# Kernel tuning notes

Measured on AMD Instinct MI355X. Metric: run time of the kernel, lower is better.

Reference implementation:

```python
import jax, jax.numpy as jnp
import numpy as np

HEADS = 8
DIM_HEAD = 32
DIM = 256           # must equal HEADS*DIM_HEAD (required by the torch view)
HIDDEN = HEADS * DIM_HEAD
NUM_GROUPS = 32
EPS = 1e-6


def setup_inputs() -> dict:
    key = jax.random.key(0)
    ks = jax.random.split(key, 6)
    b, c, h, w = 16, DIM, 64, 64
    x = jax.random.normal(ks[0], (b, c, h, w), dtype=jnp.float32)
    # conv1x1 weights stored as 2D matrices (out_ch, in_ch)
    w_qkv = jax.random.normal(ks[1], (3 * HIDDEN, DIM), dtype=jnp.float32) * (1.0 / np.sqrt(DIM))
    w_out = jax.random.normal(ks[2], (DIM, HIDDEN), dtype=jnp.float32) * (1.0 / np.sqrt(HIDDEN))
    b_out = jax.random.normal(ks[3], (DIM,), dtype=jnp.float32) * 0.01
    gn_gamma = jnp.ones((DIM,), dtype=jnp.float32)
    gn_beta = jnp.zeros((DIM,), dtype=jnp.float32)
    return {"x": x, "w_qkv": w_qkv, "w_out": w_out, "b_out": b_out,
            "gn_gamma": gn_gamma, "gn_beta": gn_beta}


def _group_norm(x, gamma, beta):
    # GroupNorm32: compute in float32, eps=1e-6, affine
    b, c, h, w = x.shape
    g = NUM_GROUPS
    xf = x.astype(jnp.float32).reshape(b, g, c // g, h, w)
    mean = xf.mean(axis=(2, 3, 4), keepdims=True)
    var = xf.var(axis=(2, 3, 4), keepdims=True)
    xn = (xf - mean) * jax.lax.rsqrt(var + EPS)
    xn = xn.reshape(b, c, h, w)
    return (xn * gamma[None, :, None, None] + beta[None, :, None, None]).astype(x.dtype)


def reference(x, w_qkv, w_out, b_out, gn_gamma, gn_beta):
    b, c, h, w = x.shape
    n = h * w
    # qkv projection (1x1 conv == matmul over channels)
    qkv = jnp.einsum('oc,bchw->bohw', w_qkv, x)            # (b, 3*hidden, h, w)
    qkv = qkv.reshape(b, 3, HEADS, DIM_HEAD, n)
    q, k, v = qkv[:, 0], qkv[:, 1], qkv[:, 2]              # (b, h, d, n)
    q = jax.nn.softmax(q, axis=-2)                         # softmax over feature dim
    k = jax.nn.softmax(k, axis=-1)                         # softmax over spatial dim
    context = jnp.einsum('bhdn,bhen->bhde', k, v)          # (b, heads, d, d)
    out = jnp.einsum('bhde,bhdn->bhen', context, q)        # (b, heads, d, n)
    out = out.reshape(b, c, h, w)
    out = jnp.einsum('oc,bchw->bohw', w_out, out) + b_out[None, :, None, None]
    out = _group_norm(out, gn_gamma, gn_beta)
    return out + x
```

## Files before the change

kernel.cpp:

```cpp
#include <hip/hip_runtime.h>


typedef short s8v __attribute__((ext_vector_type(8)));
typedef float f32x4 __attribute__((ext_vector_type(4)));

__device__ __forceinline__ short f2bf(float f) {
  union { float f; unsigned u; } v; v.f = f;
  unsigned r = v.u + 0x7FFF + ((v.u >> 16) & 1);
  return (short)(r >> 16);
}
__device__ __forceinline__ short f2bf_t(float f) {
  union { float f; unsigned u; } v; v.f = f;
  return (short)(v.u >> 16);
}
__device__ __forceinline__ float bf2f(short h) {
  union { unsigned u; float f; } v; v.u = ((unsigned)(unsigned short)h) << 16;
  return v.f;
}
__device__ __forceinline__ void gld16(const short* g, short* l) {
  __builtin_amdgcn_global_load_lds(
      (const __attribute__((address_space(1))) unsigned*)g,
      (__attribute__((address_space(3))) unsigned*)l, 16, 0, 0);
}

__global__ __launch_bounds__(256) void prep(
    const float* __restrict__ x, short* __restrict__ xt,
    const float* __restrict__ wsrc, short* __restrict__ wdst,
    float* __restrict__ st2) {
  int t = threadIdx.x;
  if (blockIdx.z == 16) {
    int slot = blockIdx.y * 64 + blockIdx.x;
    if (slot < 96) {
      int id = slot * 256 + t;
      long off = (long)id * 8;
      float4 a = *(const float4*)&wsrc[off];
      float4 b = *(const float4*)&wsrc[off + 4];
      s8v o;
      o[0] = f2bf(a.x); o[1] = f2bf(a.y); o[2] = f2bf(a.z); o[3] = f2bf(a.w);
      o[4] = f2bf(b.x); o[5] = f2bf(b.y); o[6] = f2bf(b.z); o[7] = f2bf(b.w);
      *(s8v*)&wdst[off] = o;
    } else if (slot == 96) {
      float4 z = {0.f, 0.f, 0.f, 0.f};
      ((float4*)st2)[t] = z;
    }
    return;
  }
  int b = blockIdx.z;
  int n0 = blockIdx.x * 64, c0 = blockIdx.y * 64;
  __shared__ short ls[64][65];
  const float* xb = x + ((long)b * 256 + c0) * 4096 + n0;
  int ci = t >> 4, j4 = (t & 15) * 4;
#pragma unroll
  for (int i = 0; i < 4; ++i) {
    int cl = ci + i * 16;
    float4 v = *(const float4*)&xb[(long)cl * 4096 + j4];
    ls[j4 + 0][cl] = f2bf(v.x);
    ls[j4 + 1][cl] = f2bf(v.y);
    ls[j4 + 2][cl] = f2bf(v.z);
    ls[j4 + 3][cl] = f2bf(v.w);
  }
  __syncthreads();
  short* xtb = xt + ((long)b * 4096 + n0) * 256 + c0;
#pragma unroll
  for (int i = 0; i < 2; ++i) {
    int id = t + i * 256;
    int nl = id >> 3, c8 = (id & 7) * 8;
    s8v o;
#pragma unroll
    for (int e = 0; e < 8; ++e) o[e] = ls[nl][c8 + e];
    *(s8v*)&xtb[(long)nl * 256 + c8] = o;
  }
}

__global__ __launch_bounds__(256) void gemm_qkv(
    const short* __restrict__ A, const short* __restrict__ Bt,
    short* __restrict__ kv, short* __restrict__ qT) {
  __shared__ short lA[8192];
  __shared__ short lB[8192];
  int b = blockIdx.z;
  int mt = blockIdx.y * 128, nt = blockIdx.x * 128;
  int tid = threadIdx.x;
  int lane = tid & 63;
  int wm = tid >> 7, wn = (tid >> 6) & 1;
  int rl = lane & 15, kg = lane >> 4;
  const short* Ab = A + (long)mt * 256;
  const short* Bb = Bt + ((long)b * 4096 + nt) * 256;

  f32x4 acc[4][4];
#pragma unroll
  for (int i = 0; i < 4; ++i)
#pragma unroll
    for (int j = 0; j < 4; ++j) acc[i][j] = (f32x4){0.f, 0.f, 0.f, 0.f};

  for (int k0 = 0; k0 < 256; k0 += 64) {
#pragma unroll
    for (int is = 0; is < 4; ++is) {
      int s = is * 256 + tid;
      int row = s >> 3, kcp = s & 7;
      int kcl = kcp ^ (row & 7);
      gld16(Ab + (long)row * 256 + k0 + kcl * 8, &lA[(is * 256 + (tid & ~63)) * 8]);
      gld16(Bb + (long)row * 256 + k0 + kcl * 8, &lB[(is * 256 + (tid & ~63)) * 8]);
    }
    asm volatile("s_waitcnt vmcnt(0)" ::: "memory");
    __syncthreads();
#pragma unroll
    for (int kw = 0; kw < 2; ++kw) {
      int kc = kw * 4 + kg;
      s8v av[4], bv[4];
#pragma unroll
      for (int mi = 0; mi < 4; ++mi) {
        int row = wm * 64 + mi * 16 + rl;
        av[mi] = *(const s8v*)&lA[row * 64 + ((kc ^ (row & 7)) << 3)];
      }
#pragma unroll
      for (int ni = 0; ni < 4; ++ni) {
        int row = wn * 64 + ni * 16 + rl;
        bv[ni] = *(const s8v*)&lB[row * 64 + ((kc ^ (row & 7)) << 3)];
      }
#pragma unroll
      for (int mi = 0; mi < 4; ++mi)
#pragma unroll
        for (int ni = 0; ni < 4; ++ni)
          acc[mi][ni] = __builtin_amdgcn_mfma_f32_16x16x32_bf16(
              av[mi], bv[ni], acc[mi][ni], 0, 0, 0);
    }
    __syncthreads();
  }

  if (mt < 256) {
    short* qTb = qT + ((long)b * 4096 + nt) * 256 + mt;
#pragma unroll
    for (int ni = 0; ni < 4; ++ni) {
      int n = wn * 64 + ni * 16 + rl;
#pragma unroll
      for (int p = 0; p < 2; ++p) {
        float v[8];
        float m = -1e30f;
#pragma unroll
        for (int j = 0; j < 8; ++j) {
          v[j] = acc[p * 2 + (j >> 2)][ni][j & 3];
          m = fmaxf(m, v[j]);
        }
        m = fmaxf(m, __shfl_xor(m, 16));
        m = fmaxf(m, __shfl_xor(m, 32));
        float ssum = 0.f;
#pragma unroll
        for (int j = 0; j < 8; ++j) { v[j] = __expf(v[j] - m); ssum += v[j]; }
        ssum += __shfl_xor(ssum, 16);
        ssum += __shfl_xor(ssum, 32);
        float inv = 1.f / ssum;
#pragma unroll
        for (int half = 0; half < 2; ++half) {
          short4 o;
          o.x = f2bf_t(v[half * 4 + 0] * inv);
          o.y = f2bf_t(v[half * 4 + 1] * inv);
          o.z = f2bf_t(v[half * 4 + 2] * inv);
          o.w = f2bf_t(v[half * 4 + 3] * inv);
          *(short4*)&qTb[(long)n * 256 + wm * 64 + p * 32 + half * 16 + kg * 4] = o;
        }
      }
    }
  } else {
    short* Cb = kv + ((long)b * 512 + (mt - 256)) * 4096 + nt;
#pragma unroll
    for (int mi = 0; mi < 4; ++mi) {
#pragma unroll
      for (int r = 0; r < 4; ++r) {
        int o = wm * 64 + mi * 16 + kg * 4 + r;
#pragma unroll
        for (int ni = 0; ni < 4; ++ni) {
          int n = wn * 64 + ni * 16 + rl;
          Cb[(long)o * 4096 + n] = f2bf(acc[mi][ni][r]);
        }
      }
    }
  }
}

__global__ __launch_bounds__(256) void gemm_lin(
    const short* __restrict__ A, const short* __restrict__ Bt,
    short* __restrict__ C, const float* __restrict__ bias,
    float* __restrict__ st2) {
  __shared__ short lA[8192];
  __shared__ short lB[8192];
  int b = blockIdx.z;
  int mt = blockIdx.y * 128, nt = blockIdx.x * 128;
  int tid = threadIdx.x;
  int lane = tid & 63;
  int wm = tid >> 7, wn = (tid >> 6) & 1;
  int rl = lane & 15, kg = lane >> 4;
  const short* Ab = A + (long)b * 65536 + (long)mt * 256;
  const short* Bb = Bt + ((long)b * 4096 + nt) * 256;

  f32x4 acc[4][4];
#pragma unroll
  for (int i = 0; i < 4; ++i)
#pragma unroll
    for (int j = 0; j < 4; ++j) acc[i][j] = (f32x4){0.f, 0.f, 0.f, 0.f};

  for (int k0 = 0; k0 < 256; k0 += 64) {
#pragma unroll
    for (int is = 0; is < 4; ++is) {
      int s = is * 256 + tid;
      int row = s >> 3, kcp = s & 7;
      int kcl = kcp ^ (row & 7);
      gld16(Ab + (long)row * 256 + k0 + kcl * 8, &lA[(is * 256 + (tid & ~63)) * 8]);
      gld16(Bb + (long)row * 256 + k0 + kcl * 8, &lB[(is * 256 + (tid & ~63)) * 8]);
    }
    asm volatile("s_waitcnt vmcnt(0)" ::: "memory");
    __syncthreads();
#pragma unroll
    for (int kw = 0; kw < 2; ++kw) {
      int kc = kw * 4 + kg;
      s8v av[4], bv[4];
#pragma unroll
      for (int mi = 0; mi < 4; ++mi) {
        int row = wm * 64 + mi * 16 + rl;
        av[mi] = *(const s8v*)&lA[row * 64 + ((kc ^ (row & 7)) << 3)];
      }
#pragma unroll
      for (int ni = 0; ni < 4; ++ni) {
        int row = wn * 64 + ni * 16 + rl;
        bv[ni] = *(const s8v*)&lB[row * 64 + ((kc ^ (row & 7)) << 3)];
      }
#pragma unroll
      for (int mi = 0; mi < 4; ++mi)
#pragma unroll
        for (int ni = 0; ni < 4; ++ni)
          acc[mi][ni] = __builtin_amdgcn_mfma_f32_16x16x32_bf16(
              av[mi], bv[ni], acc[mi][ni], 0, 0, 0);
    }
    __syncthreads();
  }

  short* Cb = C + ((long)b * 256 + mt) * 4096 + nt;
  float s1[4] = {0.f, 0.f, 0.f, 0.f};
  float s2[4] = {0.f, 0.f, 0.f, 0.f};
#pragma unroll
  for (int mi = 0; mi < 4; ++mi) {
#pragma unroll
    for (int r = 0; r < 4; ++r) {
      int o = wm * 64 + mi * 16 + kg * 4 + r;
      float bv = bias[mt + o];
#pragma unroll
      for (int ni = 0; ni < 4; ++ni) {
        int n = wn * 64 + ni * 16 + rl;
        short h = f2bf(acc[mi][ni][r] + bv);
        Cb[(long)o * 4096 + n] = h;
        float q = bf2f(h);
        s1[mi] += q;
        s2[mi] += q * q;
      }
    }
  }
#pragma unroll
  for (int mi = 0; mi < 4; ++mi) {
#pragma unroll
    for (int off = 1; off <= 16; off <<= 1) {
      s1[mi] += __shfl_xor(s1[mi], off);
      s2[mi] += __shfl_xor(s2[mi], off);
    }
    if (rl == 0 && (kg & 1) == 0) {
      int g = (mt >> 3) + wm * 8 + mi * 2 + (kg >> 1);
      atomicAdd(&st2[(b * 32 + g) * 2], s1[mi]);
      atomicAdd(&st2[(b * 32 + g) * 2 + 1], s2[mi]);
    }
  }
}

__global__ __launch_bounds__(256) void ctx_mfma(
    const short* __restrict__ kv, float* __restrict__ ctxp, float* __restrict__ sp) {
  int split = blockIdx.x;
  int h = blockIdx.y, b = blockIdx.z;
  int tid = threadIdx.x;
  int w = tid >> 6, l = tid & 63;
  const short* kb = kv + ((long)(b * 512) + h * 32) * 4096;
  const short* vb = kb + (long)256 * 4096;
  int rl = l & 15, kg = l >> 4;
  int n_base = split * 1024 + w * 256;

  f32x4 acc[2][2];
#pragma unroll
  for (int i = 0; i < 2; ++i)
#pragma unroll
    for (int j = 0; j < 2; ++j) acc[i][j] = (f32x4){0.f, 0.f, 0.f, 0.f};
  float s_part0 = 0.f, s_part1 = 0.f;

#pragma unroll 2
  for (int it = 0; it < 8; ++it) {
    int n0 = n_base + it * 32 + kg * 8;
    s8v a0, a1, b0, b1;
    {
      s8v kr = *(const s8v*)&kb[(long)rl * 4096 + n0];
#pragma unroll
      for (int j = 0; j < 8; ++j) {
        float f = __expf(bf2f(kr[j]));
        s_part0 += f;
        a0[j] = f2bf_t(f);
      }
    }
    {
      s8v kr = *(const s8v*)&kb[(long)(16 + rl) * 4096 + n0];
#pragma unroll
      for (int j = 0; j < 8; ++j) {
        float f = __expf(bf2f(kr[j]));
        s_part1 += f;
        a1[j] = f2bf_t(f);
      }
    }
    b0 = *(const s8v*)&vb[(long)rl * 4096 + n0];
    b1 = *(const s8v*)&vb[(long)(16 + rl) * 4096 + n0];
    acc[0][0] = __builtin_amdgcn_mfma_f32_16x16x32_bf16(a0, b0, acc[0][0], 0, 0, 0);
    acc[0][1] = __builtin_amdgcn_mfma_f32_16x16x32_bf16(a0, b1, acc[0][1], 0, 0, 0);
    acc[1][0] = __builtin_amdgcn_mfma_f32_16x16x32_bf16(a1, b0, acc[1][0], 0, 0, 0);
    acc[1][1] = __builtin_amdgcn_mfma_f32_16x16x32_bf16(a1, b1, acc[1][1], 0, 0, 0);
  }
  s_part0 += __shfl_xor(s_part0, 16); s_part0 += __shfl_xor(s_part0, 32);
  s_part1 += __shfl_xor(s_part1, 16); s_part1 += __shfl_xor(s_part1, 32);

  __shared__ float lctx[4][1024];
  __shared__ float lsum[4][32];
#pragma unroll
  for (int di = 0; di < 2; ++di)
#pragma unroll
    for (int ei = 0; ei < 2; ++ei)
#pragma unroll
      for (int r = 0; r < 4; ++r) {
        int row = di * 16 + kg * 4 + r;
        int col = ei * 16 + rl;
        lctx[w][row * 32 + col] = acc[di][ei][r];
      }
  if (kg == 0) { lsum[w][rl] = s_part0; lsum[w][16 + rl] = s_part1; }
  __syncthreads();
  long base = (long)(b * 8 + h) * 4 + split;
#pragma unroll
  for (int i = 0; i < 4; ++i) {
    int id = tid + i * 256;
    ctxp[base * 1024 + id] = lctx[0][id] + lctx[1][id] + lctx[2][id] + lctx[3][id];
  }
  if (tid < 32)
    sp[base * 32 + tid] = lsum[0][tid] + lsum[1][tid] + lsum[2][tid] + lsum[3][tid];
}

__global__ __launch_bounds__(256) void make_wf(
    const float* __restrict__ ctxp, const float* __restrict__ sp,
    const float* __restrict__ w_out, short* __restrict__ wf) {
  int h = blockIdx.x, b = blockIdx.y;
  __shared__ float c[32][33];
  __shared__ float inv_s[32];
  __shared__ float wv[256][33];
  int t = threadIdx.x;
  long base = (long)(b * 8 + h) * 4;
#pragma unroll
  for (int i = 0; i < 4; ++i) {
    int id = t + i * 256;
    float v = ctxp[base * 1024 + id] + ctxp[(base + 1) * 1024 + id] +
              ctxp[(base + 2) * 1024 + id] + ctxp[(base + 3) * 1024 + id];
    c[id >> 5][id & 31] = v;
  }
  if (t < 32) {
    float sv = sp[base * 32 + t] + sp[(base + 1) * 32 + t] +
               sp[(base + 2) * 32 + t] + sp[(base + 3) * 32 + t];
    inv_s[t] = 1.f / sv;
  }
#pragma unroll
  for (int r = 0; r < 32; ++r) {
    int row = r * 8 + (t >> 5);
    wv[row][t & 31] = w_out[row * 256 + h * 32 + (t & 31)];
  }
  __syncthreads();
  float wr[32];
#pragma unroll
  for (int e = 0; e < 32; ++e) wr[e] = wv[t][e];
  float tmp[32];
#pragma unroll
  for (int dd = 0; dd < 32; ++dd) {
    float sum = 0.f;
#pragma unroll
    for (int e = 0; e < 32; ++e) sum += wr[e] * c[dd][e];
    tmp[dd] = sum * inv_s[dd];
  }
  short* dst = wf + ((long)b * 256 + t) * 256 + h * 32;
#pragma unroll
  for (int c8 = 0; c8 < 4; ++c8) {
    s8v o;
#pragma unroll
    for (int e = 0; e < 8; ++e) o[e] = f2bf(tmp[c8 * 8 + e]);
    *(s8v*)&dst[c8 * 8] = o;
  }
}

__global__ __launch_bounds__(256) void final_out(
    const short* __restrict__ lin, const float* __restrict__ x,
    const float2* __restrict__ st2, const float* __restrict__ gamma,
    const float* __restrict__ beta, float* __restrict__ out) {
  long id = (long)blockIdx.x * 256 + threadIdx.x;
  long e0 = id * 8;
  int b = (int)(e0 >> 20);
  int rem = (int)(e0 & 1048575);
  int c = rem >> 12;
  float2 st = st2[b * 32 + (c >> 3)];
  float mean = st.x * (1.f / 32768.f);
  float inv = rsqrtf(st.y * (1.f / 32768.f) - mean * mean + 1e-6f);
  float ga = gamma[c] * inv;
  float be = beta[c] - mean * ga;
  s8v l8 = __builtin_nontemporal_load((const s8v*)&lin[e0]);
  f32x4 x0 = __builtin_nontemporal_load((const f32x4*)&x[e0]);
  f32x4 x1 = __builtin_nontemporal_load((const f32x4*)&x[e0 + 4]);
  f32x4 o0, o1;
  o0[0] = bf2f(l8[0]) * ga + be + x0[0];
  o0[1] = bf2f(l8[1]) * ga + be + x0[1];
  o0[2] = bf2f(l8[2]) * ga + be + x0[2];
  o0[3] = bf2f(l8[3]) * ga + be + x0[3];
  o1[0] = bf2f(l8[4]) * ga + be + x1[0];
  o1[1] = bf2f(l8[5]) * ga + be + x1[1];
  o1[2] = bf2f(l8[6]) * ga + be + x1[2];
  o1[3] = bf2f(l8[7]) * ga + be + x1[3];
  __builtin_nontemporal_store(o0, (f32x4*)&out[e0]);
  __builtin_nontemporal_store(o1, (f32x4*)&out[e0 + 4]);
}

extern "C" void kernel_launch(void* const* d_in, const int* in_sizes, int n_in,
                              void* d_out, int out_size, void* d_ws, size_t ws_size,
                              hipStream_t stream) {
  const float* x     = (const float*)d_in[0];
  const float* w_qkv = (const float*)d_in[1];
  const float* w_out = (const float*)d_in[2];
  const float* b_out = (const float*)d_in[3];
  const float* gamma = (const float*)d_in[4];
  const float* beta  = (const float*)d_in[5];
  float* out = (float*)d_out;

  short* xt   = (short*)d_ws;
  short* qT   = xt + 16777216;
  short* kvb  = qT + 16777216;
  short* lin  = kvb + 33554432;
  short* wqb  = lin + 16777216;
  short* wfb  = wqb + 196608;
  float* ctxp = (float*)(wfb + 1048576);
  float* sp   = ctxp + 524288;
  float* st2  = sp + 16384;

  prep<<<dim3(64, 4, 17), 256, 0, stream>>>(x, xt, w_qkv, wqb, st2);
  gemm_qkv<<<dim3(32, 6, 16), 256, 0, stream>>>(wqb, xt, kvb, qT);
  ctx_mfma<<<dim3(4, 8, 16), 256, 0, stream>>>(kvb, ctxp, sp);
  make_wf<<<dim3(8, 16), 256, 0, stream>>>(ctxp, sp, w_out, wfb);
  gemm_lin<<<dim3(32, 2, 16), 256, 0, stream>>>(wfb, qT, lin, b_out, st2);
  final_out<<<8192, 256, 0, stream>>>(lin, x, (const float2*)st2, gamma, beta, out);
}
```

Before: 145.9 us.

## Fuse make_wf into ctx_mfma via last-block-done atomic counter

Removes the separate make_wf launch by having the last of the four split blocks per (batch, head) in ctx_mfma perform the context reduction and the weight fold. Completion is detected with a per-head atomic counter that prep zeroes, with thread fences around it. This saves one kernel launch and its gap, at the cost of a larger shared-memory footprint in ctx_mfma (about 38 KB) and a serialized tail on the last block.

```diff
diff --git a/kernel.cpp b/kernel.cpp
--- a/kernel.cpp
+++ b/kernel.cpp
@@ -26,7 +26,7 @@
 __global__ __launch_bounds__(256) void prep(
     const float* __restrict__ x, short* __restrict__ xt,
     const float* __restrict__ wsrc, short* __restrict__ wdst,
-    float* __restrict__ st2) {
+    float* __restrict__ st2, int* __restrict__ cnt) {
   int t = threadIdx.x;
   if (blockIdx.z == 16) {
     int slot = blockIdx.y * 64 + blockIdx.x;
@@ -42,6 +42,7 @@
     } else if (slot == 96) {
       float4 z = {0.f, 0.f, 0.f, 0.f};
       ((float4*)st2)[t] = z;
+      if (t < 32) ((float4*)cnt)[t] = z;
     }
     return;
   }
@@ -269,7 +270,10 @@
 }
 
 __global__ __launch_bounds__(256) void ctx_mfma(
-    const short* __restrict__ kv, float* __restrict__ ctxp, float* __restrict__ sp) {
+    const short* __restrict__ kv, float* __restrict__ ctxp, float* __restrict__ sp,
+    const float* __restrict__ w_out, short* __restrict__ wf, int* __restrict__ cnt) {
+  __shared__ float sh[9536];
+  __shared__ int lastf;
   int split = blockIdx.x;
   int h = blockIdx.y, b = blockIdx.z;
   int tid = threadIdx.x;
@@ -318,8 +322,8 @@
   s_part0 += __shfl_xor(s_part0, 16); s_part0 += __shfl_xor(s_part0, 32);
   s_part1 += __shfl_xor(s_part1, 16); s_part1 += __shfl_xor(s_part1, 32);
 
-  __shared__ float lctx[4][1024];
-  __shared__ float lsum[4][32];
+  float* lctx = sh;
+  float* lsum = sh + 4096;
 #pragma unroll
   for (int di = 0; di < 2; ++di)
 #pragma unroll
@@ -328,59 +332,63 @@
       for (int r = 0; r < 4; ++r) {
         int row = di * 16 + kg * 4 + r;
         int col = ei * 16 + rl;
-        lctx[w][row * 32 + col] = acc[di][ei][r];
-      }
-  if (kg == 0) { lsum[w][rl] = s_part0; lsum[w][16 + rl] = s_part1; }
+        lctx[w * 1024 + row * 32 + col] = acc[di][ei][r];
+      }
+  if (kg == 0) { lsum[w * 32 + rl] = s_part0; lsum[w * 32 + 16 + rl] = s_part1; }
   __syncthreads();
   long base = (long)(b * 8 + h) * 4 + split;
 #pragma unroll
   for (int i = 0; i < 4; ++i) {
     int id = tid + i * 256;
-    ctxp[base * 1024 + id] = lctx[0][id] + lctx[1][id] + lctx[2][id] + lctx[3][id];
+    ctxp[base * 1024 + id] = lctx[id] + lctx[1024 + id] + lctx[2048 + id] + lctx[3072 + id];
   }
   if (tid < 32)
-    sp[base * 32 + tid] = lsum[0][tid] + lsum[1][tid] + lsum[2][tid] + lsum[3][tid];
-}
-
-__global__ __launch_bounds__(256) void make_wf(
-    const float* __restrict__ ctxp, const float* __restrict__ sp,
-    const float* __restrict__ w_out, short* __restrict__ wf) {
-  int h = blockIdx.x, b = blockIdx.y;
-  __shared__ float c[32][33];
-  __shared__ float inv_s[32];
-  __shared__ float wv[256][33];
-  int t = threadIdx.x;
-  long base = (long)(b * 8 + h) * 4;
+    sp[base * 32 + tid] = lsum[tid] + lsum[32 + tid] + lsum[64 + tid] + lsum[96 + tid];
+
+  __threadfence();
+  __syncthreads();
+  if (tid == 0) {
+    int old = atomicAdd(&cnt[b * 8 + h], 1);
+    lastf = (old == 3);
+  }
+  __syncthreads();
+  if (!lastf) return;
+  __threadfence();
+
+  float* c     = sh;
+  float* inv_s = sh + 1056;
+  float* wv    = sh + 1088;
+  long wbase = (long)(b * 8 + h) * 4;
 #pragma unroll
   for (int i = 0; i < 4; ++i) {
-    int id = t + i * 256;
-    float v = ctxp[base * 1024 + id] + ctxp[(base + 1) * 1024 + id] +
-              ctxp[(base + 2) * 1024 + id] + ctxp[(base + 3) * 1024 + id];
-    c[id >> 5][id & 31] = v;
-  }
-  if (t < 32) {
-    float sv = sp[base * 32 + t] + sp[(base + 1) * 32 + t] +
-               sp[(base + 2) * 32 + t] + sp[(base + 3) * 32 + t];
-    inv_s[t] = 1.f / sv;
+    int id = tid + i * 256;
+    float v = ctxp[wbase * 1024 + id] + ctxp[(wbase + 1) * 1024 + id] +
+              ctxp[(wbase + 2) * 1024 + id] + ctxp[(wbase + 3) * 1024 + id];
+    c[(id >> 5) * 33 + (id & 31)] = v;
+  }
+  if (tid < 32) {
+    float sv = sp[wbase * 32 + tid] + sp[(wbase + 1) * 32 + tid] +
+               sp[(wbase + 2) * 32 + tid] + sp[(wbase + 3) * 32 + tid];
+    inv_s[tid] = 1.f / sv;
   }
 #pragma unroll
   for (int r = 0; r < 32; ++r) {
-    int row = r * 8 + (t >> 5);
-    wv[row][t & 31] = w_out[row * 256 + h * 32 + (t & 31)];
+    int row = r * 8 + (tid >> 5);
+    wv[row * 33 + (tid & 31)] = w_out[row * 256 + h * 32 + (tid & 31)];
   }
   __syncthreads();
   float wr[32];
 #pragma unroll
-  for (int e = 0; e < 32; ++e) wr[e] = wv[t][e];
+  for (int e = 0; e < 32; ++e) wr[e] = wv[tid * 33 + e];
   float tmp[32];
 #pragma unroll
   for (int dd = 0; dd < 32; ++dd) {
     float sum = 0.f;
 #pragma unroll
-    for (int e = 0; e < 32; ++e) sum += wr[e] * c[dd][e];
+    for (int e = 0; e < 32; ++e) sum += wr[e] * c[dd * 33 + e];
     tmp[dd] = sum * inv_s[dd];
   }
-  short* dst = wf + ((long)b * 256 + t) * 256 + h * 32;
+  short* dst = wf + ((long)b * 256 + tid) * 256 + h * 32;
 #pragma unroll
   for (int c8 = 0; c8 < 4; ++c8) {
     s8v o;
@@ -440,11 +448,11 @@
   float* ctxp = (float*)(wfb + 1048576);
   float* sp   = ctxp + 524288;
   float* st2  = sp + 16384;
-
-  prep<<<dim3(64, 4, 17), 256, 0, stream>>>(x, xt, w_qkv, wqb, st2);
+  int*   cnt  = (int*)(st2 + 1024);
+
+  prep<<<dim3(64, 4, 17), 256, 0, stream>>>(x, xt, w_qkv, wqb, st2, cnt);
   gemm_qkv<<<dim3(32, 6, 16), 256, 0, stream>>>(wqb, xt, kvb, qT);
-  ctx_mfma<<<dim3(4, 8, 16), 256, 0, stream>>>(kvb, ctxp, sp);
-  make_wf<<<dim3(8, 16), 256, 0, stream>>>(ctxp, sp, w_out, wfb);
+  ctx_mfma<<<dim3(4, 8, 16), 256, 0, stream>>>(kvb, ctxp, sp, w_out, wfb, cnt);
   gemm_lin<<<dim3(32, 2, 16), 256, 0, stream>>>(wfb, qT, lin, b_out, st2);
   final_out<<<8192, 256, 0, stream>>>(lin, x, (const float2*)st2, gamma, beta, out);
 }
```

Result: slower. 215.7 us (+47.9%).

## Double-buffer LDS in QKV GEMM to overlap global loads with MFMA

Applied to the files above, without the earlier changes.

Splits the K loop of the QKV projection GEMM into 32-wide steps with two ping-pong LDS buffers. The next step's global-to-LDS loads are issued before computing on the current buffer, with partial vmcnt waits, so memory latency can hide behind MFMA work. The swizzle is narrowed to 4 chunks per row to match the smaller tile. This adds more barriers per K step and relies on hand-counted vmcnt values being correct.

```diff
diff --git a/kernel.cpp b/kernel.cpp
--- a/kernel.cpp
+++ b/kernel.cpp
@@ -75,8 +75,8 @@
 __global__ __launch_bounds__(256) void gemm_qkv(
     const short* __restrict__ A, const short* __restrict__ Bt,
     short* __restrict__ kv, short* __restrict__ qT) {
-  __shared__ short lA[8192];
-  __shared__ short lB[8192];
+  __shared__ short lA[2][4096];
+  __shared__ short lB[2][4096];
   int b = blockIdx.z;
   int mt = blockIdx.y * 128, nt = blockIdx.x * 128;
   int tid = threadIdx.x;
@@ -92,39 +92,48 @@
 #pragma unroll
     for (int j = 0; j < 4; ++j) acc[i][j] = (f32x4){0.f, 0.f, 0.f, 0.f};
 
-  for (int k0 = 0; k0 < 256; k0 += 64) {
-#pragma unroll
-    for (int is = 0; is < 4; ++is) {
+  auto stage = [&](int buf, int k0) {
+#pragma unroll
+    for (int is = 0; is < 2; ++is) {
       int s = is * 256 + tid;
-      int row = s >> 3, kcp = s & 7;
-      int kcl = kcp ^ (row & 7);
-      gld16(Ab + (long)row * 256 + k0 + kcl * 8, &lA[(is * 256 + (tid & ~63)) * 8]);
-      gld16(Bb + (long)row * 256 + k0 + kcl * 8, &lB[(is * 256 + (tid & ~63)) * 8]);
-    }
-    asm volatile("s_waitcnt vmcnt(0)" ::: "memory");
-    __syncthreads();
-#pragma unroll
-    for (int kw = 0; kw < 2; ++kw) {
-      int kc = kw * 4 + kg;
-      s8v av[4], bv[4];
-#pragma unroll
-      for (int mi = 0; mi < 4; ++mi) {
-        int row = wm * 64 + mi * 16 + rl;
-        av[mi] = *(const s8v*)&lA[row * 64 + ((kc ^ (row & 7)) << 3)];
-      }
-#pragma unroll
-      for (int ni = 0; ni < 4; ++ni) {
-        int row = wn * 64 + ni * 16 + rl;
-        bv[ni] = *(const s8v*)&lB[row * 64 + ((kc ^ (row & 7)) << 3)];
-      }
-#pragma unroll
-      for (int mi = 0; mi < 4; ++mi)
-#pragma unroll
-        for (int ni = 0; ni < 4; ++ni)
-          acc[mi][ni] = __builtin_amdgcn_mfma_f32_16x16x32_bf16(
-              av[mi], bv[ni], acc[mi][ni], 0, 0, 0);
-    }
-    __syncthreads();
+      int row = s >> 2, kcp = s & 3;
+      int kcl = kcp ^ (row & 3);
+      gld16(Ab + (long)row * 256 + k0 + kcl * 8, &lA[buf][(is * 256 + (tid & ~63)) * 8]);
+      gld16(Bb + (long)row * 256 + k0 + kcl * 8, &lB[buf][(is * 256 + (tid & ~63)) * 8]);
+    }
+  };
+
+  stage(0, 0);
+#pragma unroll
+  for (int s = 0; s < 8; ++s) {
+    int cur = s & 1;
+    if (s < 7) {
+      stage(cur ^ 1, (s + 1) * 32);
+      asm volatile("s_waitcnt vmcnt(4)" ::: "memory");
+    } else {
+      asm volatile("s_waitcnt vmcnt(0)" ::: "memory");
+    }
+    __builtin_amdgcn_s_barrier();
+    int kc = kg;
+    s8v av[4], bv[4];
+#pragma unroll
+    for (int mi = 0; mi < 4; ++mi) {
+      int row = wm * 64 + mi * 16 + rl;
+      av[mi] = *(const s8v*)&lA[cur][row * 32 + ((kc ^ (row & 3)) << 3)];
+    }
+#pragma unroll
+    for (int ni = 0; ni < 4; ++ni) {
+      int row = wn * 64 + ni * 16 + rl;
+      bv[ni] = *(const s8v*)&lB[cur][row * 32 + ((kc ^ (row & 3)) << 3)];
+    }
+#pragma unroll
+    for (int mi = 0; mi < 4; ++mi)
+#pragma unroll
+      for (int ni = 0; ni < 4; ++ni)
+        acc[mi][ni] = __builtin_amdgcn_mfma_f32_16x16x32_bf16(
+            av[mi], bv[ni], acc[mi][ni], 0, 0, 0);
+    asm volatile("s_waitcnt lgkmcnt(0)" ::: "memory");
+    __builtin_amdgcn_s_barrier();
   }
 
   if (mt < 256) {
```

Result: slower. 155.1 us (+6.3%).
